# Optimization experiments

Hardware: AMD Instinct MI355X
Metric: run time of the kernel (lower is better)

Reference implementation:

```python
import jax, jax.numpy as jnp
import numpy as np

WINDOW_SIZE = 11
SIGMA = 1.5
C1 = 0.01 ** 2
C2 = 0.03 ** 2


def _gaussian_1d(window_size, sigma):
    x = np.arange(window_size, dtype=np.float32)
    g = np.exp(-((x - window_size // 2) ** 2) / (2.0 * sigma ** 2))
    g = g / g.sum()
    return jnp.asarray(g, dtype=jnp.float32)


def _blur(x, g1d):
    # Separable depthwise Gaussian blur, SAME padding.
    # x: [B, C, H, W]; mathematically identical to conv with outer(g, g).
    c = x.shape[1]
    pad = WINDOW_SIZE // 2
    kh = jnp.broadcast_to(g1d.reshape(1, 1, WINDOW_SIZE, 1), (c, 1, WINDOW_SIZE, 1))
    kw = jnp.broadcast_to(g1d.reshape(1, 1, 1, WINDOW_SIZE), (c, 1, 1, WINDOW_SIZE))
    dn = ('NCHW', 'OIHW', 'NCHW')
    x = jax.lax.conv_general_dilated(x, kh, (1, 1), [(pad, pad), (0, 0)],
                                     dimension_numbers=dn, feature_group_count=c)
    x = jax.lax.conv_general_dilated(x, kw, (1, 1), [(0, 0), (pad, pad)],
                                     dimension_numbers=dn, feature_group_count=c)
    return x


def setup_inputs() -> dict:
    key = jax.random.key(0)
    k1, k2 = jax.random.split(key)
    shape = (32, 1, 512, 512)
    img1 = jax.random.uniform(k1, shape, dtype=jnp.float32)
    img2 = jax.random.uniform(k2, shape, dtype=jnp.float32)
    return {"img1": img1, "img2": img2}


def reference(img1, img2):
    g1d = _gaussian_1d(WINDOW_SIZE, SIGMA)
    mu1 = _blur(img1, g1d)
    mu2 = _blur(img2, g1d)
    mu1_sq = mu1 * mu1
    mu2_sq = mu2 * mu2
    mu1_mu2 = mu1 * mu2
    sigma1_sq = _blur(img1 * img1, g1d) - mu1_sq
    sigma2_sq = _blur(img2 * img2, g1d) - mu2_sq
    sigma12 = _blur(img1 * img2, g1d) - mu1_mu2
    ssim_map = ((2.0 * mu1_mu2 + C1) * (2.0 * sigma12 + C2)) / (
        (mu1_sq + mu2_sq + C1) * (sigma1_sq + sigma2_sq + C2))
    return ssim_map.mean()  # size_average=True
```

## Files before the change

kernel.cpp:

```cpp
#include <hip/hip_runtime.h>

#define HH 512
#define WW 512
#define BATCH 32
#define BH 16
#define NB (HH / BH)
#define TPB 256
#define NBLOCKS (NB * BATCH)
#define PW 528
#define CBASE 0xAAAAAAAAu


typedef float f2 __attribute__((ext_vector_type(2)));

#define VERT(ACC, O)                                                          \
  do {                                                                        \
    _Pragma("unroll")                                                         \
    for (int a = 0; a < 5; ++a) {                                             \
      ACC[a][0] = f2{0.f, 0.f};                                               \
      ACC[a][1] = f2{0.f, 0.f};                                               \
    }                                                                         \
    _Pragma("unroll")                                                         \
    for (int e = 0; e < 12; ++e) {                                            \
      const f2 g2 = f2{(e < 11) ? G[e] : 0.f, (e > 0) ? G[e - 1] : 0.f};      \
      const float xv[2] = {w1[(O) + e].x, w1[(O) + e].y};                     \
      const float yv[2] = {w2[(O) + e].x, w2[(O) + e].y};                     \
      _Pragma("unroll")                                                       \
      for (int i = 0; i < 2; ++i) {                                           \
        const float x = xv[i], y = yv[i];                                     \
        const float xx = x * x, yy = y * y, xy = x * y;                       \
        ACC[0][i] = __builtin_elementwise_fma(g2, f2{x, x}, ACC[0][i]);       \
        ACC[1][i] = __builtin_elementwise_fma(g2, f2{y, y}, ACC[1][i]);       \
        ACC[2][i] = __builtin_elementwise_fma(g2, f2{xx, xx}, ACC[2][i]);     \
        ACC[3][i] = __builtin_elementwise_fma(g2, f2{yy, yy}, ACC[3][i]);     \
        ACC[4][i] = __builtin_elementwise_fma(g2, f2{xy, xy}, ACC[4][i]);     \
      }                                                                       \
    }                                                                         \
  } while (0)

#define STORE_ACC(ACC)                                                        \
  do {                                                                        \
    _Pragma("unroll")                                                         \
    for (int a = 0; a < 5; ++a) {                                             \
      float* base = sp + a * (2 * PW) + 4 * tid + 18;        \
      *(f2*)(base) = ACC[a][0];                                               \
      *(f2*)(base + 2) = ACC[a][1];                                           \
    }                                                                         \
  } while (0)

__global__ __launch_bounds__(TPB) void ssim_main(
    const float* __restrict__ img1,
    const float* __restrict__ img2,
    unsigned* __restrict__ counter,
    float* __restrict__ partial,
    float* __restrict__ out)
{
  constexpr float G[11] = {
      0.00102838f, 0.00759876f, 0.03600077f, 0.10936070f, 0.21300553f,
      0.26601171f,
      0.21300553f, 0.10936070f, 0.03600077f, 0.00759876f, 0.00102838f};
  constexpr float C1 = 1.0e-4f;
  constexpr float C2 = 9.0e-4f;

  const int tid  = threadIdx.x;
  const int band = blockIdx.x;
  const int bat  = blockIdx.y;
  const int r0   = band * BH;
  const float* p1 = img1 + (size_t)bat * (HH * WW);
  const float* p2 = img2 + (size_t)bat * (HH * WW);
  const int c0 = tid * 2;

  __shared__ __align__(16) float sp[5 * PW * 2];

  if (tid < 80) {
    const int a = tid >> 4, s = tid & 15;
    const int idx = (s < 9) ? s : (512 + s);
    *(f2*)(sp + a * (2 * PW) + 2 * idx) = f2{0.f, 0.f};
  }

  float2 w1[14], w2[14];
#pragma unroll
  for (int j = 0; j < 14; ++j) {
    const int r = r0 - 5 + j;
    float2 a = make_float2(0.f, 0.f), b = a;
    if (r >= 0 && r < HH) {
      a = *(const float2*)(p1 + r * WW + c0);
      b = *(const float2*)(p2 + r * WW + c0);
    }
    w1[j] = a; w2[j] = b;
  }

  {
    f2 accC[5][2];
    VERT(accC, 0);
    STORE_ACC(accC);
  }

  float ssum = 0.f;

#pragma unroll 1
  for (int q = 0; q < BH; q += 2) {
    __syncthreads();

    float2 ta1 = make_float2(0.f, 0.f), ta2 = ta1, tb1 = ta1, tb2 = ta1;
    if (q + 4 < BH) {
      const int ra = r0 + q + 9;
      const int rb = r0 + q + 10;
      if (ra < HH) {
        ta1 = *(const float2*)(p1 + ra * WW + c0);
        ta2 = *(const float2*)(p2 + ra * WW + c0);
      }
      if (rb < HH) {
        tb1 = *(const float2*)(p1 + rb * WW + c0);
        tb2 = *(const float2*)(p2 + rb * WW + c0);
      }
    }

    f2 h2[5][2];
#pragma unroll
    for (int a = 0; a < 5; ++a) {
      const float* base = sp + a * (2 * PW);
      f2 t2[12];
#pragma unroll
      for (int m = 0; m < 6; ++m) {
        const float4 X = *(const float4*)(base + 4 * tid + 8 + 4 * m);
        t2[2 * m]     = f2{X.x, X.y};
        t2[2 * m + 1] = f2{X.z, X.w};
      }
#pragma unroll
      for (int j = 0; j < 2; ++j) {
        f2 hv = f2{0.f, 0.f};
#pragma unroll
        for (int k = 0; k < 11; ++k)
          hv = __builtin_elementwise_fma(f2{G[k], G[k]}, t2[j + k], hv);
        h2[a][j] = hv;
      }
    }

    f2 accN[5][2];
    if (q + 2 < BH) {
      VERT(accN, 2);
    }

#pragma unroll
    for (int j = 0; j < 2; ++j) {
      const f2 mu1 = h2[0][j], mu2 = h2[1][j];
      const f2 mu12 = mu1 * mu2;
      const f2 den1 = __builtin_elementwise_fma(
          mu1, mu1, __builtin_elementwise_fma(mu2, mu2, f2{C1, C1}));
      const f2 vs   = (h2[2][j] + h2[3][j]) - den1 + f2{C1 + C2, C1 + C2};
      const f2 sg12 = h2[4][j] - mu12;
      const f2 num = (mu12 + mu12 + f2{C1, C1}) * (sg12 + sg12 + f2{C2, C2});
      const f2 den = den1 * vs;
      float rn0 = __builtin_amdgcn_rcpf(den.x);
      float rn1 = __builtin_amdgcn_rcpf(den.y);
      rn0 = rn0 * fmaf(-den.x, rn0, 2.0f);
      rn1 = rn1 * fmaf(-den.y, rn1, 2.0f);
      ssum = fmaf(num.x, rn0, ssum);
      ssum = fmaf(num.y, rn1, ssum);
    }

    __syncthreads();

    if (q + 2 < BH) {
      STORE_ACC(accN);
    }

#pragma unroll
    for (int j = 0; j < 12; ++j) { w1[j] = w1[j + 2]; w2[j] = w2[j + 2]; }
    w1[12] = ta1; w2[12] = ta2;
    w1[13] = tb1; w2[13] = tb2;
  }

#pragma unroll
  for (int off = 32; off > 0; off >>= 1) ssum += __shfl_xor(ssum, off, 64);
  float*  wred = sp;
  double* dred = (double*)(sp + 8);
  int*    flag = (int*)(sp + 16);
  const int wid = tid >> 6;
  if ((tid & 63) == 0) wred[wid] = ssum;
  __syncthreads();
  if (tid == 0) {
    const float bsum = wred[0] + wred[1] + wred[2] + wred[3];
    atomicExch(&partial[bat * NB + band], bsum);
    __threadfence();
    const unsigned old = atomicAdd(counter, 1u);
    flag[0] = (old == CBASE + (unsigned)NBLOCKS - 1u) ? 1 : 0;
  }
  __syncthreads();
  if (flag[0]) {
    double s = 0.0;
    for (int i = tid; i < NBLOCKS; i += TPB)
      s += (double)atomicAdd(&partial[i], 0.0f);
#pragma unroll
    for (int off = 32; off > 0; off >>= 1) s += __shfl_xor(s, off, 64);
    if ((tid & 63) == 0) dred[wid] = s;
    __syncthreads();
    if (tid == 0)
      out[0] = (float)((dred[0] + dred[1] + dred[2] + dred[3]) /
                       (double)((size_t)BATCH * HH * WW));
  }
}

extern "C" void kernel_launch(void* const* d_in, const int* in_sizes, int n_in,
                              void* d_out, int out_size, void* d_ws, size_t ws_size,
                              hipStream_t stream) {
  const float* img1 = (const float*)d_in[0];
  const float* img2 = (const float*)d_in[1];
  float* out = (float*)d_out;
  unsigned* counter = (unsigned*)d_ws;
  float* partial = (float*)((char*)d_ws + 16);
  dim3 grid(NB, BATCH);
  ssim_main<<<grid, TPB, 0, stream>>>(img1, img2, counter, partial, out);
}
```

Baseline: 131.1 us.

## Merge x²+y² blur channel and process four rows per barrier pair

Cuts the blurred channels from five to four by blurring x²+y² as one quantity, since only sigma1²+sigma2² is needed. The loop now handles four output rows per iteration with two shared-memory buffers, which halves the number of barriers. It also swaps __syncthreads for a custom lgkmcnt-wait barrier. In exchange it raises register pressure from two sets of vertical accumulators and prefetching four rows, and the single summed channel may change rounding slightly.

```diff
diff --git a/kernel.cpp b/kernel.cpp
--- a/kernel.cpp
+++ b/kernel.cpp
@@ -4,10 +4,13 @@
 #define WW 512
 #define BATCH 32
 #define BH 16
+#define PH 4
 #define NB (HH / BH)
 #define TPB 256
 #define NBLOCKS (NB * BATCH)
 #define PW 528
+#define ABUF (PW * 2)
+#define BUFF (4 * ABUF)
 #define CBASE 0xAAAAAAAAu
 
 
@@ -16,7 +19,7 @@
 #define VERT(ACC, O)                                                          \
   do {                                                                        \
     _Pragma("unroll")                                                         \
-    for (int a = 0; a < 5; ++a) {                                             \
+    for (int a = 0; a < 4; ++a) {                                             \
       ACC[a][0] = f2{0.f, 0.f};                                               \
       ACC[a][1] = f2{0.f, 0.f};                                               \
     }                                                                         \
@@ -28,24 +31,22 @@
       _Pragma("unroll")                                                       \
       for (int i = 0; i < 2; ++i) {                                           \
         const float x = xv[i], y = yv[i];                                     \
-        const float xx = x * x, yy = y * y, xy = x * y;                       \
+        const float s = fmaf(y, y, x * x);                                    \
+        const float p = x * y;                                                \
         ACC[0][i] = __builtin_elementwise_fma(g2, f2{x, x}, ACC[0][i]);       \
         ACC[1][i] = __builtin_elementwise_fma(g2, f2{y, y}, ACC[1][i]);       \
-        ACC[2][i] = __builtin_elementwise_fma(g2, f2{xx, xx}, ACC[2][i]);     \
-        ACC[3][i] = __builtin_elementwise_fma(g2, f2{yy, yy}, ACC[3][i]);     \
-        ACC[4][i] = __builtin_elementwise_fma(g2, f2{xy, xy}, ACC[4][i]);     \
+        ACC[2][i] = __builtin_elementwise_fma(g2, f2{s, s}, ACC[2][i]);       \
+        ACC[3][i] = __builtin_elementwise_fma(g2, f2{p, p}, ACC[3][i]);       \
       }                                                                       \
     }                                                                         \
   } while (0)
 
-#define STORE_ACC(ACC)                                                        \
+#define RAW_BARRIER()                                                         \
   do {                                                                        \
-    _Pragma("unroll")                                                         \
-    for (int a = 0; a < 5; ++a) {                                             \
-      float* base = sp + a * (2 * PW) + 4 * tid + 18;        \
-      *(f2*)(base) = ACC[a][0];                                               \
-      *(f2*)(base + 2) = ACC[a][1];                                           \
-    }                                                                         \
+    __builtin_amdgcn_sched_barrier(0);                                        \
+    asm volatile("s_waitcnt lgkmcnt(0)");                                     \
+    __builtin_amdgcn_s_barrier();                                             \
+    __builtin_amdgcn_sched_barrier(0);                                        \
   } while (0)
 
 __global__ __launch_bounds__(TPB) void ssim_main(
@@ -70,12 +71,12 @@
   const float* p2 = img2 + (size_t)bat * (HH * WW);
   const int c0 = tid * 2;
 
-  __shared__ __align__(16) float sp[5 * PW * 2];
-
-  if (tid < 80) {
+  __shared__ __align__(16) float sp[2 * BUFF];
+
+  if (tid < 128) {
     const int a = tid >> 4, s = tid & 15;
     const int idx = (s < 9) ? s : (512 + s);
-    *(f2*)(sp + a * (2 * PW) + 2 * idx) = f2{0.f, 0.f};
+    *(f2*)(sp + a * ABUF + 2 * idx) = f2{0.f, 0.f};
   }
 
   float2 w1[14], w2[14];
@@ -90,86 +91,88 @@
     w1[j] = a; w2[j] = b;
   }
 
-  {
-    f2 accC[5][2];
-    VERT(accC, 0);
-    STORE_ACC(accC);
-  }
-
   float ssum = 0.f;
 
 #pragma unroll 1
-  for (int q = 0; q < BH; q += 2) {
-    __syncthreads();
-
-    float2 ta1 = make_float2(0.f, 0.f), ta2 = ta1, tb1 = ta1, tb2 = ta1;
-    if (q + 4 < BH) {
-      const int ra = r0 + q + 9;
-      const int rb = r0 + q + 10;
-      if (ra < HH) {
-        ta1 = *(const float2*)(p1 + ra * WW + c0);
-        ta2 = *(const float2*)(p2 + ra * WW + c0);
+  for (int q = 0; q < BH; q += PH) {
+    float2 tp1[4], tp2[4];
+#pragma unroll
+    for (int m = 0; m < 4; ++m) { tp1[m] = make_float2(0.f, 0.f); tp2[m] = tp1[m]; }
+    if (q + PH < BH) {
+#pragma unroll
+      for (int m = 0; m < 4; ++m) {
+        const int r = r0 + q + 9 + m;
+        if (r < HH) {
+          tp1[m] = *(const float2*)(p1 + r * WW + c0);
+          tp2[m] = *(const float2*)(p2 + r * WW + c0);
+        }
       }
-      if (rb < HH) {
-        tb1 = *(const float2*)(p1 + rb * WW + c0);
-        tb2 = *(const float2*)(p2 + rb * WW + c0);
+    }
+
+    f2 accA[4][2], accB[4][2];
+    VERT(accA, 0);
+    VERT(accB, 2);
+
+#pragma unroll
+    for (int a = 0; a < 4; ++a) {
+      float* b0 = sp + a * ABUF + 4 * tid + 18;
+      *(f2*)(b0)        = accA[a][0];
+      *(f2*)(b0 + 2)    = accA[a][1];
+      float* b1 = b0 + BUFF;
+      *(f2*)(b1)        = accB[a][0];
+      *(f2*)(b1 + 2)    = accB[a][1];
+    }
+
+    RAW_BARRIER();
+
+#pragma unroll
+    for (int pr = 0; pr < 2; ++pr) {
+      f2 h2[4][2];
+#pragma unroll
+      for (int a = 0; a < 4; ++a) {
+        const float* base = sp + pr * BUFF + a * ABUF;
+        f2 t2[12];
+#pragma unroll
+        for (int m = 0; m < 6; ++m) {
+          const float4 X = *(const float4*)(base + 4 * tid + 8 + 4 * m);
+          t2[2 * m]     = f2{X.x, X.y};
+          t2[2 * m + 1] = f2{X.z, X.w};
+        }
+#pragma unroll
+        for (int j = 0; j < 2; ++j) {
+          f2 hv = f2{0.f, 0.f};
+#pragma unroll
+          for (int k = 0; k < 11; ++k)
+            hv = __builtin_elementwise_fma(f2{G[k], G[k]}, t2[j + k], hv);
+          h2[a][j] = hv;
+        }
       }
-    }
-
-    f2 h2[5][2];
-#pragma unroll
-    for (int a = 0; a < 5; ++a) {
-      const float* base = sp + a * (2 * PW);
-      f2 t2[12];
-#pragma unroll
-      for (int m = 0; m < 6; ++m) {
-        const float4 X = *(const float4*)(base + 4 * tid + 8 + 4 * m);
-        t2[2 * m]     = f2{X.x, X.y};
-        t2[2 * m + 1] = f2{X.z, X.w};
+#pragma unroll
+      for (int j = 0; j < 2; ++j) {
+        const f2 mu1 = h2[0][j], mu2 = h2[1][j];
+        const f2 S   = h2[2][j], P   = h2[3][j];
+        const f2 mu12 = mu1 * mu2;
+        const f2 den1 = __builtin_elementwise_fma(
+            mu1, mu1, __builtin_elementwise_fma(mu2, mu2, f2{C1, C1}));
+        const f2 vs   = S - den1 + f2{C1 + C2, C1 + C2};
+        const f2 sg12 = P - mu12;
+        const f2 num = (mu12 + mu12 + f2{C1, C1}) * (sg12 + sg12 + f2{C2, C2});
+        const f2 den = den1 * vs;
+        float rn0 = __builtin_amdgcn_rcpf(den.x);
+        float rn1 = __builtin_amdgcn_rcpf(den.y);
+        rn0 = rn0 * fmaf(-den.x, rn0, 2.0f);
+        rn1 = rn1 * fmaf(-den.y, rn1, 2.0f);
+        ssum = fmaf(num.x, rn0, ssum);
+        ssum = fmaf(num.y, rn1, ssum);
       }
-#pragma unroll
-      for (int j = 0; j < 2; ++j) {
-        f2 hv = f2{0.f, 0.f};
-#pragma unroll
-        for (int k = 0; k < 11; ++k)
-          hv = __builtin_elementwise_fma(f2{G[k], G[k]}, t2[j + k], hv);
-        h2[a][j] = hv;
-      }
-    }
-
-    f2 accN[5][2];
-    if (q + 2 < BH) {
-      VERT(accN, 2);
-    }
-
-#pragma unroll
-    for (int j = 0; j < 2; ++j) {
-      const f2 mu1 = h2[0][j], mu2 = h2[1][j];
-      const f2 mu12 = mu1 * mu2;
-      const f2 den1 = __builtin_elementwise_fma(
-          mu1, mu1, __builtin_elementwise_fma(mu2, mu2, f2{C1, C1}));
-      const f2 vs   = (h2[2][j] + h2[3][j]) - den1 + f2{C1 + C2, C1 + C2};
-      const f2 sg12 = h2[4][j] - mu12;
-      const f2 num = (mu12 + mu12 + f2{C1, C1}) * (sg12 + sg12 + f2{C2, C2});
-      const f2 den = den1 * vs;
-      float rn0 = __builtin_amdgcn_rcpf(den.x);
-      float rn1 = __builtin_amdgcn_rcpf(den.y);
-      rn0 = rn0 * fmaf(-den.x, rn0, 2.0f);
-      rn1 = rn1 * fmaf(-den.y, rn1, 2.0f);
-      ssum = fmaf(num.x, rn0, ssum);
-      ssum = fmaf(num.y, rn1, ssum);
-    }
-
-    __syncthreads();
-
-    if (q + 2 < BH) {
-      STORE_ACC(accN);
-    }
-
-#pragma unroll
-    for (int j = 0; j < 12; ++j) { w1[j] = w1[j + 2]; w2[j] = w2[j + 2]; }
-    w1[12] = ta1; w2[12] = ta2;
-    w1[13] = tb1; w2[13] = tb2;
+    }
+
+    RAW_BARRIER();
+
+#pragma unroll
+    for (int j = 0; j < 10; ++j) { w1[j] = w1[j + 4]; w2[j] = w2[j + 4]; }
+#pragma unroll
+    for (int m = 0; m < 4; ++m) { w1[10 + m] = tp1[m]; w2[10 + m] = tp2[m]; }
   }
 
 #pragma unroll
```

Result: no change. 128.7 us (-1.8%).
